# Performance work log

Hardware: AMD Instinct MI355X
Metric: run time of the kernel (lower is better)

Reference implementation:

```python
import jax, jax.numpy as jnp
import numpy as np

EPS = 1e-6
NUM_GROUPS = 32


def setup_inputs() -> dict:
    key = jax.random.key(0)
    ks = jax.random.split(key, 10)
    b, c, h, w = 8, 256, 128, 128
    x = jax.random.normal(ks[0], (b, c, h, w), dtype=jnp.float32)
    gamma = jnp.ones((c,), dtype=jnp.float32)
    beta = jnp.zeros((c,), dtype=jnp.float32)
    Wq = jax.random.normal(ks[1], (c, c), dtype=jnp.float32) * 0.02
    bq = jnp.zeros((c,), dtype=jnp.float32)
    Wk = jax.random.normal(ks[2], (c, c), dtype=jnp.float32) * 0.02
    bk = jnp.zeros((c,), dtype=jnp.float32)
    Wv = jax.random.normal(ks[3], (c, c), dtype=jnp.float32) * 0.02
    bv = jnp.zeros((c,), dtype=jnp.float32)
    Wo = jax.random.normal(ks[4], (c, c), dtype=jnp.float32) * 0.02
    bo = jnp.zeros((c,), dtype=jnp.float32)
    return {"x": x, "gamma": gamma, "beta": beta, "Wq": Wq, "bq": bq,
            "Wk": Wk, "bk": bk, "Wv": Wv, "bv": bv, "Wo": Wo, "bo": bo}


def _group_norm(x, gamma, beta):
    b, c, h, w = x.shape
    g = NUM_GROUPS
    xg = x.reshape(b, g, c // g, h, w)
    mean = jnp.mean(xg, axis=(2, 3, 4), keepdims=True)
    var = jnp.var(xg, axis=(2, 3, 4), keepdims=True)
    xn = ((xg - mean) * jax.lax.rsqrt(var + EPS)).reshape(b, c, h, w)
    return xn * gamma[None, :, None, None] + beta[None, :, None, None]


def reference(x, gamma, beta, Wq, bq, Wk, bk, Wv, bv, Wo, bo):
    b, c, h, w = x.shape
    xn = _group_norm(x, gamma, beta)
    xf = xn.reshape(b, c, h * w)  # [b, c, n]
    # 1x1 convs == channel-mixing matmuls
    Q = jnp.einsum('oc,bcn->bon', Wq, xf) + bq[None, :, None]
    K = jnp.einsum('oc,bcn->bon', Wk, xf) + bk[None, :, None]
    V = jnp.einsum('oc,bcn->bon', Wv, xf) + bv[None, :, None]
    # softmax over the spatial dim n (linear-attention variant)
    Q = jax.nn.softmax(Q, axis=-1)
    K = jax.nn.softmax(K, axis=-1)
    attn = jnp.einsum('bcn,bdn->bcd', Q, K) / jnp.sqrt(jnp.float32(c))  # [b, c, c]
    out = jnp.einsum('bcd,bdn->bcn', attn, V)  # [b, c, n]
    out = jnp.einsum('oc,bcn->bon', Wo, out) + bo[None, :, None]
    return out.reshape(b, c, h, w)
```

## Files before the change

kernel.cpp:

```cpp
#include <hip/hip_runtime.h>
#include <hip/hip_bf16.h>

#define BATCH 8
#define CHN 256
#define HWN 16384
#define EPSV 1e-6f
#define ESCH 32

typedef __attribute__((ext_vector_type(8))) short bf16x8;
typedef __attribute__((ext_vector_type(4))) short s16x4;
typedef __attribute__((ext_vector_type(4))) float f32x4;
typedef __hip_bfloat16 bf16;

__device__ __forceinline__ short f2s(float f){
  union { bf16 h; short s; } u; u.h = __float2bfloat16(f); return u.s;
}
__device__ __forceinline__ float s2f(short s){
  union { unsigned u; float f; } v; v.u = ((unsigned)(unsigned short)s) << 16; return v.f;
}
__device__ __forceinline__ void gload16(const bf16* g, bf16* l){
  __builtin_amdgcn_global_load_lds((const __attribute__((address_space(1))) void*)g,
                                   (__attribute__((address_space(3))) void*)l, 16, 0, 0);
}

__global__ __launch_bounds__(256) void xstats_t(const float* __restrict__ x,
    bf16* __restrict__ xt, float* __restrict__ pst){
  int b = blockIdx.y, n0 = blockIdx.x * 64;
  __shared__ bf16 tile[256][70];
  __shared__ float sg[32], ssg[32];
  int t = threadIdx.x;
  if (t < 32){ sg[t] = 0.f; ssg[t] = 0.f; }
  __syncthreads();
  const float* xb = x + (size_t)b * CHN * HWN;
  #pragma unroll 4
  for (int i = 0; i < 16; i++){
    int c = i * 16 + (t >> 4);
    int nf = (t & 15) * 4;
    float4 v = *(const float4*)(xb + (size_t)c * HWN + n0 + nf);
    tile[c][nf + 0] = __float2bfloat16(v.x);
    tile[c][nf + 1] = __float2bfloat16(v.y);
    tile[c][nf + 2] = __float2bfloat16(v.z);
    tile[c][nf + 3] = __float2bfloat16(v.w);
    float s  = v.x + v.y + v.z + v.w;
    float ss = v.x*v.x + v.y*v.y + v.z*v.z + v.w*v.w;
    s  += __shfl_xor(s, 1);  s  += __shfl_xor(s, 2);
    s  += __shfl_xor(s, 4);  s  += __shfl_xor(s, 8);
    ss += __shfl_xor(ss, 1); ss += __shfl_xor(ss, 2);
    ss += __shfl_xor(ss, 4); ss += __shfl_xor(ss, 8);
    if ((t & 15) == 0){ atomicAdd(&sg[c >> 3], s); atomicAdd(&ssg[c >> 3], ss); }
  }
  __syncthreads();
  bf16* o = xt + (size_t)b * HWN * CHN;
  #pragma unroll 4
  for (int j = 0; j < 64; j++)
    o[(size_t)(n0 + j) * CHN + t] = tile[t][j];
  if (t < 32){
    atomicAdd(&pst[(b * 32 + t) * 2],     sg[t]);
    atomicAdd(&pst[(b * 32 + t) * 2 + 1], ssg[t]);
  }
}

__global__ __launch_bounds__(256) void wprep(const float* __restrict__ Wq,
    const float* __restrict__ Wk, const float* __restrict__ Wv,
    const float* __restrict__ Wo, const float* __restrict__ gamma,
    const float* __restrict__ beta, const float* __restrict__ bv,
    const float* __restrict__ pst, bf16* __restrict__ wqk,
    bf16* __restrict__ wvt, bf16* __restrict__ wob, float* __restrict__ tvb){
  int w = blockIdx.x, b = blockIdx.y, rt = blockIdx.z, t = threadIdx.x;
  if (w == 3 && b != 0) return;
  const float* W = (w == 0) ? Wq : ((w == 1) ? Wk : ((w == 2) ? Wv : Wo));
  __shared__ float a_s[256], sh_s[256];
  __shared__ float racc[16];
  {
    int bg = b * 32 + (t >> 3);
    float m   = pst[bg * 2] * (1.f / 131072.f);
    float var = pst[bg * 2 + 1] * (1.f / 131072.f) - m * m;
    float r = rsqrtf(var + EPSV);
    float a = r * gamma[t];
    a_s[t] = a;
    sh_s[t] = beta[t] - m * a;
  }
  if (t < 16) racc[t] = 0.f;
  __syncthreads();
  float mya = a_s[t], mysh = sh_s[t];
  int lane = t & 63;
  bf16* wo_qk = wqk + ((size_t)b << 17) + ((size_t)w << 16);
  bf16* wo_v  = wvt + ((size_t)b << 16);
  #pragma unroll
  for (int jj = 0; jj < 16; jj++){
    int j = rt * 16 + jj;
    float wv_ = W[j * 256 + t];
    if (w < 2) wo_qk[j * 256 + t] = __float2bfloat16(wv_ * mya);
    else if (w == 3) wob[j * 256 + t] = __float2bfloat16(wv_);
    else {
      wo_v[(size_t)t * 256 + j] = __float2bfloat16(wv_ * mya);
      float p = wv_ * mysh;
      p += __shfl_xor(p, 1);  p += __shfl_xor(p, 2);  p += __shfl_xor(p, 4);
      p += __shfl_xor(p, 8);  p += __shfl_xor(p, 16); p += __shfl_xor(p, 32);
      if (lane == 0) atomicAdd(&racc[jj], p);
    }
  }
  if (w == 2){
    __syncthreads();
    if (t < 16) tvb[b * 256 + rt * 16 + t] = racc[t] + bv[rt * 16 + t];
  }
}

__global__ __launch_bounds__(256, 2) void qk_gemm(const bf16* __restrict__ wqk,
    const bf16* __restrict__ xt, bf16* __restrict__ Eout,
    float* __restrict__ sums){
  __shared__ bf16 lW[2][512 * 32];
  __shared__ bf16 lX[2][64 * 32];
  int t = threadIdx.x, nt = blockIdx.x, b = blockIdx.y;
  const bf16* Wb = wqk + ((size_t)b << 17);
  const bf16* Xb = xt + (size_t)b * HWN * CHN + (size_t)(nt * 64) * CHN;
  int lane = t & 63, w = t >> 6, r = lane & 15, kc = lane >> 4;
  f32x4 acc[4][8] = {};

  auto stage = [&](int buf, int k0){
    #pragma unroll
    for (int rep = 0; rep < 8; rep++){
      int c = t + rep * 256; int row = c >> 2;
      int off = ((c & 3) ^ ((c >> 3) & 3)) * 8;
      gload16(Wb + (size_t)row * 256 + k0 + off, &lW[buf][c * 8]);
    }
    { int row = t >> 2;
      int off = ((t & 3) ^ ((t >> 3) & 3)) * 8;
      gload16(Xb + (size_t)row * 256 + k0 + off, &lX[buf][t * 8]); }
  };

  stage(0, 0);
  __syncthreads();
  int cur = 0;
  int slot8 = (kc ^ ((r >> 1) & 3)) * 8;
  for (int ks = 0; ks < 8; ks++){
    if (ks < 7) stage(cur ^ 1, (ks + 1) * 32);
    bf16x8 af[4], bfv[8];
    #pragma unroll
    for (int i = 0; i < 4; i++)
      af[i] = *(const bf16x8*)&lX[cur][(i * 16 + r) * 32 + slot8];
    #pragma unroll
    for (int f = 0; f < 8; f++)
      bfv[f] = *(const bf16x8*)&lW[cur][(w * 128 + f * 16 + r) * 32 + slot8];
    #pragma unroll
    for (int i = 0; i < 4; i++)
      #pragma unroll
      for (int f = 0; f < 8; f++)
        acc[i][f] = __builtin_amdgcn_mfma_f32_16x16x32_bf16(af[i], bfv[f], acc[i][f], 0, 0, 0);
    __syncthreads();
    cur ^= 1;
  }

  char* scrB = (char*)&lW[0][0];
  float colp[8];
  #pragma unroll
  for (int f = 0; f < 8; f++) colp[f] = 0.f;
  #pragma unroll
  for (int f = 0; f < 8; f++){
    int wrow = w * 128 + f * 16 + r;
    int key = (wrow & 7) << 4;
    #pragma unroll
    for (int i = 0; i < 4; i++){
      s16x4 pk;
      #pragma unroll
      for (int j = 0; j < 4; j++){
        float e = __expf(acc[i][f][j]);
        colp[f] += e;
        pk[j] = f2s(e);
      }
      int nb0 = (i * 16 + kc * 4) * 2;
      *(s16x4*)(scrB + wrow * 128 + (nb0 ^ key)) = pk;
    }
  }
  #pragma unroll
  for (int f = 0; f < 8; f++){
    float v = colp[f];
    v += __shfl_xor(v, 16); v += __shfl_xor(v, 32);
    if (lane < 16){
      int wrow = w * 128 + f * 16 + r;
      int sidx = wrow < 256 ? b * 256 + wrow : 2048 + b * 256 + (wrow - 256);
      atomicAdd(&sums[sidx], v);
    }
  }
  __syncthreads();
  #pragma unroll
  for (int pass = 0; pass < 16; pass++){
    int c = t + pass * 256;
    int row = c >> 3, q = c & 7;
    int key = (row & 7) << 4;
    int4 v = *(const int4*)(scrB + row * 128 + ((q * 16) ^ key));
    size_t ridx = row < 256 ? (size_t)(b * 256 + row)
                            : (size_t)(2048 + b * 256 + row - 256);
    *(int4*)&Eout[ridx * HWN + nt * 64 + q * 8] = v;
  }
}

__global__ __launch_bounds__(256, 2) void es_gemm(const bf16* __restrict__ Ek,
    const bf16* __restrict__ Eq, float* __restrict__ spart){
  __shared__ bf16 lA[2][128 * 32];
  __shared__ bf16 lB[2][256 * 32];
  int t = threadIdx.x, ch = blockIdx.x, mt = blockIdx.y, z = blockIdx.z;
  const bf16* At = Ek + (size_t)z * 256 * HWN + (size_t)(mt * 128) * HWN + ch * 512;
  const bf16* Bt = Eq + (size_t)z * 256 * HWN + ch * 512;
  f32x4 acc[4][8] = {};
  int lane = t & 63, w = t >> 6, r = lane & 15, kc = lane >> 4;
  int ng = w >> 1, cg = w & 1;

  auto stage = [&](int buf, int k0){
    #pragma unroll
    for (int rep = 0; rep < 2; rep++){
      int c = t + rep * 256; int row = c >> 2;
      int off = ((c & 3) ^ ((c >> 3) & 3)) * 8;
      gload16(At + (size_t)row * HWN + k0 + off, &lA[buf][c * 8]);
    }
    #pragma unroll
    for (int rep = 0; rep < 4; rep++){
      int c = t + rep * 256; int row = c >> 2;
      int off = ((c & 3) ^ ((c >> 3) & 3)) * 8;
      gload16(Bt + (size_t)row * HWN + k0 + off, &lB[buf][c * 8]);
    }
  };

  stage(0, 0);
  __syncthreads();
  int cur = 0;
  int slot8 = (kc ^ ((r >> 1) & 3)) * 8;
  for (int ks = 0; ks < 16; ks++){
    if (ks < 15) stage(cur ^ 1, (ks + 1) * 32);
    bf16x8 af[4], bfv[8];
    #pragma unroll
    for (int i = 0; i < 4; i++)
      af[i] = *(const bf16x8*)&lA[cur][(ng * 64 + i * 16 + r) * 32 + slot8];
    #pragma unroll
    for (int f = 0; f < 8; f++)
      bfv[f] = *(const bf16x8*)&lB[cur][(cg * 128 + f * 16 + r) * 32 + slot8];
    #pragma unroll
    for (int i = 0; i < 4; i++)
      #pragma unroll
      for (int f = 0; f < 8; f++)
        acc[i][f] = __builtin_amdgcn_mfma_f32_16x16x32_bf16(af[i], bfv[f], acc[i][f], 0, 0, 0);
    __syncthreads();
    cur ^= 1;
  }

  float* sp = spart + ((size_t)(z * ESCH + ch) << 16);
  #pragma unroll
  for (int f = 0; f < 8; f++){
    int q = cg * 128 + f * 16 + r;
    #pragma unroll
    for (int i = 0; i < 4; i++){
      int k0i = mt * 128 + ng * 64 + i * 16 + kc * 4;
      *(f32x4*)&sp[q * 256 + k0i] = acc[i][f];
    }
  }
}

__global__ void reduce_S(const float* __restrict__ sp, float* __restrict__ S){
  size_t i = ((size_t)blockIdx.x * 256 + threadIdx.x) * 4;
  size_t b = i >> 16, cd = i & 65535;
  float4 s = {0.f, 0.f, 0.f, 0.f};
  #pragma unroll
  for (int ch = 0; ch < ESCH; ch++){
    float4 v = *(const float4*)&sp[((b * ESCH + ch) << 16) + cd];
    s.x += v.x; s.y += v.y; s.z += v.z; s.w += v.w;
  }
  *(float4*)&S[i] = s;
}

__global__ __launch_bounds__(256) void scaleS_t(const float* __restrict__ S,
    const float* __restrict__ sums, bf16* __restrict__ T1t){
  int id = blockIdx.x, b = blockIdx.y;
  int dt = id >> 2, ct = id & 3, t = threadIdx.x;
  __shared__ float tile[64][65];
  __shared__ float sq_s[64], sk_s[64];
  if (t < 64)       sq_s[t]      = 0.0625f / sums[b * 256 + ct * 64 + t];
  else if (t < 128) sk_s[t - 64] = 1.f / sums[2048 + b * 256 + dt * 64 + (t - 64)];
  const float* Sb = S + ((size_t)b << 16);
  #pragma unroll
  for (int i = 0; i < 4; i++){
    int c_l = i * 16 + (t >> 4);
    int d_l0 = (t & 15) * 4;
    float4 v = *(const float4*)&Sb[(size_t)(ct * 64 + c_l) * 256 + dt * 64 + d_l0];
    tile[d_l0 + 0][c_l] = v.x;
    tile[d_l0 + 1][c_l] = v.y;
    tile[d_l0 + 2][c_l] = v.z;
    tile[d_l0 + 3][c_l] = v.w;
  }
  __syncthreads();
  bf16* Tb = T1t + ((size_t)b << 16);
  #pragma unroll
  for (int i = 0; i < 4; i++){
    int d_l = i * 16 + (t >> 4);
    int c_l0 = (t & 15) * 4;
    s16x4 pk;
    #pragma unroll
    for (int jj = 0; jj < 4; jj++)
      pk[jj] = f2s(tile[d_l][c_l0 + jj] * sq_s[c_l0 + jj] * sk_s[d_l]);
    *(s16x4*)&Tb[(size_t)(dt * 64 + d_l) * 256 + ct * 64 + c_l0] = pk;
  }
}

__global__ __launch_bounds__(256, 2) void nt_gemm(const bf16* __restrict__ A,
    const bf16* __restrict__ B, bf16* __restrict__ out,
    long Asb, long Bsb, long Osb){
  __shared__ bf16 lA[2][256 * 32];
  __shared__ bf16 lB[2][128 * 32];
  int t = threadIdx.x, mt = blockIdx.x, b = blockIdx.y;
  const bf16* Ab = A + (size_t)b * Asb;
  const bf16* Bb = B + (size_t)b * Bsb + (size_t)(mt * 128) * 256;
  bf16* Ob = out + (size_t)b * Osb + (size_t)(mt * 128) * 256;
  int lane = t & 63, w = t >> 6, r = lane & 15, kc = lane >> 4;
  f32x4 acc[16][2] = {};

  auto stage = [&](int buf, int k0){
    #pragma unroll
    for (int rep = 0; rep < 4; rep++){
      int c = t + rep * 256; int row = c >> 2, off = (c & 3) * 8;
      gload16(Ab + (size_t)row * 256 + k0 + off, &lA[buf][c * 8]);
    }
    #pragma unroll
    for (int rep = 0; rep < 2; rep++){
      int c = t + rep * 256; int row = c >> 2, off = (c & 3) * 8;
      gload16(Bb + (size_t)row * 256 + k0 + off, &lB[buf][c * 8]);
    }
  };

  stage(0, 0);
  __syncthreads();
  int cur = 0;
  for (int ks = 0; ks < 8; ks++){
    if (ks < 7) stage(cur ^ 1, (ks + 1) * 32);
    bf16x8 bfv[2];
    #pragma unroll
    for (int f = 0; f < 2; f++)
      bfv[f] = *(const bf16x8*)&lB[cur][(w * 32 + f * 16 + r) * 32 + kc * 8];
    #pragma unroll
    for (int i = 0; i < 16; i++){
      bf16x8 af = *(const bf16x8*)&lA[cur][(i * 16 + r) * 32 + kc * 8];
      acc[i][0] = __builtin_amdgcn_mfma_f32_16x16x32_bf16(af, bfv[0], acc[i][0], 0, 0, 0);
      acc[i][1] = __builtin_amdgcn_mfma_f32_16x16x32_bf16(af, bfv[1], acc[i][1], 0, 0, 0);
    }
    __syncthreads();
    cur ^= 1;
  }

  #pragma unroll
  for (int f = 0; f < 2; f++){
    int bcol = w * 32 + f * 16 + r;
    #pragma unroll
    for (int i = 0; i < 16; i++){
      s16x4 pk;
      #pragma unroll
      for (int j = 0; j < 4; j++) pk[j] = f2s(acc[i][f][j]);
      *(s16x4*)&Ob[(size_t)bcol * 256 + i * 16 + kc * 4] = pk;
    }
  }
}

__global__ __launch_bounds__(256) void beff_k(const bf16* __restrict__ Mbf,
    const float* __restrict__ tvb, const float* __restrict__ bo,
    float* __restrict__ beff){
  int b = blockIdx.x, t = threadIdx.x;
  __shared__ float tv[256];
  tv[t] = tvb[b * 256 + t];
  __syncthreads();
  const bf16* Mr = Mbf + ((size_t)b << 16) + (size_t)t * 256;
  float s = 0.f;
  #pragma unroll
  for (int k = 0; k < 32; k++){
    bf16x8 v = *(const bf16x8*)&Mr[k * 8];
    #pragma unroll
    for (int e = 0; e < 8; e++) s += s2f(v[e]) * tv[k * 8 + e];
  }
  beff[b * 256 + t] = s + bo[t];
}

__global__ __launch_bounds__(256, 2) void out_gemm(const bf16* __restrict__ xt,
    const bf16* __restrict__ Nb, const float* __restrict__ beff,
    float* __restrict__ out){
  __shared__ bf16 lA[2][128 * 32];
  __shared__ bf16 lB[2][256 * 32];
  int t = threadIdx.x, nt = blockIdx.x, z = blockIdx.y;
  const bf16* At = xt + (size_t)z * HWN * CHN + (size_t)(nt * 128) * CHN;
  const bf16* Bt = Nb + (size_t)z * 65536;
  f32x4 acc[4][8] = {};
  int lane = t & 63, w = t >> 6, r = lane & 15, kc = lane >> 4;
  int ng = w >> 1, cg = w & 1;

  auto stage = [&](int buf, int k0){
    #pragma unroll
    for (int rep = 0; rep < 2; rep++){
      int c = t + rep * 256; int row = c >> 2;
      int off = ((c & 3) ^ ((c >> 3) & 3)) * 8;
      gload16(At + (size_t)row * 256 + k0 + off, &lA[buf][c * 8]);
    }
    #pragma unroll
    for (int rep = 0; rep < 4; rep++){
      int c = t + rep * 256; int row = c >> 2;
      int off = ((c & 3) ^ ((c >> 3) & 3)) * 8;
      gload16(Bt + (size_t)row * 256 + k0 + off, &lB[buf][c * 8]);
    }
  };

  stage(0, 0);
  __syncthreads();
  int cur = 0;
  int slot8 = (kc ^ ((r >> 1) & 3)) * 8;
  for (int ks = 0; ks < 8; ks++){
    if (ks < 7) stage(cur ^ 1, (ks + 1) * 32);
    bf16x8 af[4], bfv[8];
    #pragma unroll
    for (int i = 0; i < 4; i++)
      af[i] = *(const bf16x8*)&lA[cur][(ng * 64 + i * 16 + r) * 32 + slot8];
    #pragma unroll
    for (int f = 0; f < 8; f++)
      bfv[f] = *(const bf16x8*)&lB[cur][(cg * 128 + f * 16 + r) * 32 + slot8];
    #pragma unroll
    for (int i = 0; i < 4; i++)
      #pragma unroll
      for (int f = 0; f < 8; f++)
        acc[i][f] = __builtin_amdgcn_mfma_f32_16x16x32_bf16(af[i], bfv[f], acc[i][f], 0, 0, 0);
    __syncthreads();
    cur ^= 1;
  }

  float* ob = out + (size_t)z * CHN * HWN;
  #pragma unroll
  for (int f = 0; f < 8; f++){
    int o = cg * 128 + f * 16 + r;
    float bb = beff[z * 256 + o];
    #pragma unroll
    for (int i = 0; i < 4; i++){
      int n0 = nt * 128 + ng * 64 + i * 16 + kc * 4;
      float4 st = { acc[i][f][0] + bb, acc[i][f][1] + bb,
                    acc[i][f][2] + bb, acc[i][f][3] + bb };
      *(float4*)&ob[(size_t)o * HWN + n0] = st;
    }
  }
}

extern "C" void kernel_launch(void* const* d_in, const int* in_sizes, int n_in,
                              void* d_out, int out_size, void* d_ws, size_t ws_size,
                              hipStream_t stream){
  const float* x     = (const float*)d_in[0];
  const float* gamma = (const float*)d_in[1];
  const float* beta  = (const float*)d_in[2];
  const float* Wq    = (const float*)d_in[3];
  const float* Wk    = (const float*)d_in[5];
  const float* Wv    = (const float*)d_in[7];
  const float* bv    = (const float*)d_in[8];
  const float* Wo    = (const float*)d_in[9];
  const float* bo    = (const float*)d_in[10];

  char* ws = (char*)d_ws;
  bf16*  xt    = (bf16*) (ws + 0);
  float* spart = (float*)(ws + 67108864);
  bf16*  wqk   = (bf16*) (ws + 134217728);
  bf16*  wob   = (bf16*) (ws + 136314880);
  bf16*  wvt   = (bf16*) (ws + 136445952);
  float* S     = (float*)(ws + 137494528);
  bf16*  T1t   = (bf16*) (ws + 139591680);
  bf16*  Mbf   = (bf16*) (ws + 140640256);
  bf16*  Nb    = (bf16*) (ws + 141688832);
  float* sums  = (float*)(ws + 142737408);
  float* pst   = (float*)(ws + 142753792);
  float* tvb   = (float*)(ws + 142755840);
  float* beff  = (float*)(ws + 142764032);

  bf16* Qb = (bf16*)d_out;
  bf16* Kb = Qb + (size_t)2048 * HWN;

  hipMemsetAsync(sums, 0, 4096 * sizeof(float), stream);
  hipMemsetAsync(pst,  0,  512 * sizeof(float), stream);

  xstats_t<<<dim3(256, 8), dim3(256), 0, stream>>>(x, xt, pst);
  wprep<<<dim3(4, 8, 16), dim3(256), 0, stream>>>(Wq, Wk, Wv, Wo, gamma, beta,
                                                  bv, pst, wqk, wvt, wob, tvb);
  qk_gemm<<<dim3(256, 8), dim3(256), 0, stream>>>(wqk, xt, Qb, sums);
  es_gemm<<<dim3(ESCH, 2, 8), dim3(256), 0, stream>>>(Kb, Qb, spart);
  reduce_S<<<dim3(512), dim3(256), 0, stream>>>(spart, S);
  scaleS_t<<<dim3(16, 8), dim3(256), 0, stream>>>(S, sums, T1t);
  nt_gemm<<<dim3(2, 8), dim3(256), 0, stream>>>(T1t, wob, Mbf, 65536L, 0L, 65536L);
  beff_k<<<dim3(8), dim3(256), 0, stream>>>(Mbf, tvb, bo, beff);
  nt_gemm<<<dim3(2, 8), dim3(256), 0, stream>>>(wvt, Mbf, Nb, 65536L, 65536L, 65536L);
  out_gemm<<<dim3(128, 8), dim3(256), 0, stream>>>(xt, Nb, beff, (float*)d_out);
}
```

Baseline: 310.5 us.

## Retile qk_gemm to 256x128 blocks split over Q/K halves

The Q/K projection GEMM changes from a 512-row weight by 64-column spatial tile to a 256-row (one of Q or K) by 128-column tile, with Q/K selected by a new grid dimension. Shared memory shrinks, and each block loads half the weight per step while reusing it over twice as many spatial columns. The aim is to cut redundant weight traffic and use an LDS footprint better suited to occupancy. The exp/store epilogue becomes two passes through a smaller scratch buffer with extra barriers, and the sums atomics map to the new row layout.

```diff
diff --git a/kernel.cpp b/kernel.cpp
--- a/kernel.cpp
+++ b/kernel.cpp
@@ -109,24 +109,27 @@
 __global__ __launch_bounds__(256, 2) void qk_gemm(const bf16* __restrict__ wqk,
     const bf16* __restrict__ xt, bf16* __restrict__ Eout,
     float* __restrict__ sums){
-  __shared__ bf16 lW[2][512 * 32];
-  __shared__ bf16 lX[2][64 * 32];
-  int t = threadIdx.x, nt = blockIdx.x, b = blockIdx.y;
-  const bf16* Wb = wqk + ((size_t)b << 17);
-  const bf16* Xb = xt + (size_t)b * HWN * CHN + (size_t)(nt * 64) * CHN;
+  __shared__ bf16 lW[2][256 * 32];
+  __shared__ bf16 lX[2][128 * 32];
+  int t = threadIdx.x, nt = blockIdx.x, h = blockIdx.y, b = blockIdx.z;
+  const bf16* Wb = wqk + ((size_t)b << 17) + ((size_t)h << 16);
+  const bf16* Xb = xt + (size_t)b * HWN * CHN + (size_t)(nt * 128) * CHN;
   int lane = t & 63, w = t >> 6, r = lane & 15, kc = lane >> 4;
-  f32x4 acc[4][8] = {};
+  f32x4 acc[8][4] = {};
 
   auto stage = [&](int buf, int k0){
     #pragma unroll
-    for (int rep = 0; rep < 8; rep++){
+    for (int rep = 0; rep < 4; rep++){
       int c = t + rep * 256; int row = c >> 2;
       int off = ((c & 3) ^ ((c >> 3) & 3)) * 8;
       gload16(Wb + (size_t)row * 256 + k0 + off, &lW[buf][c * 8]);
     }
-    { int row = t >> 2;
-      int off = ((t & 3) ^ ((t >> 3) & 3)) * 8;
-      gload16(Xb + (size_t)row * 256 + k0 + off, &lX[buf][t * 8]); }
+    #pragma unroll
+    for (int rep = 0; rep < 2; rep++){
+      int c = t + rep * 256; int row = c >> 2;
+      int off = ((c & 3) ^ ((c >> 3) & 3)) * 8;
+      gload16(Xb + (size_t)row * 256 + k0 + off, &lX[buf][c * 8]);
+    }
   };
 
   stage(0, 0);
@@ -135,63 +138,62 @@
   int slot8 = (kc ^ ((r >> 1) & 3)) * 8;
   for (int ks = 0; ks < 8; ks++){
     if (ks < 7) stage(cur ^ 1, (ks + 1) * 32);
-    bf16x8 af[4], bfv[8];
-    #pragma unroll
-    for (int i = 0; i < 4; i++)
+    bf16x8 af[8], bfv[4];
+    #pragma unroll
+    for (int i = 0; i < 8; i++)
       af[i] = *(const bf16x8*)&lX[cur][(i * 16 + r) * 32 + slot8];
     #pragma unroll
-    for (int f = 0; f < 8; f++)
-      bfv[f] = *(const bf16x8*)&lW[cur][(w * 128 + f * 16 + r) * 32 + slot8];
-    #pragma unroll
-    for (int i = 0; i < 4; i++)
+    for (int f = 0; f < 4; f++)
+      bfv[f] = *(const bf16x8*)&lW[cur][(w * 64 + f * 16 + r) * 32 + slot8];
+    #pragma unroll
+    for (int i = 0; i < 8; i++)
       #pragma unroll
-      for (int f = 0; f < 8; f++)
+      for (int f = 0; f < 4; f++)
         acc[i][f] = __builtin_amdgcn_mfma_f32_16x16x32_bf16(af[i], bfv[f], acc[i][f], 0, 0, 0);
     __syncthreads();
     cur ^= 1;
   }
 
   char* scrB = (char*)&lW[0][0];
-  float colp[8];
-  #pragma unroll
-  for (int f = 0; f < 8; f++) colp[f] = 0.f;
-  #pragma unroll
-  for (int f = 0; f < 8; f++){
-    int wrow = w * 128 + f * 16 + r;
-    int key = (wrow & 7) << 4;
-    #pragma unroll
-    for (int i = 0; i < 4; i++){
-      s16x4 pk;
+  float colp[4] = {0.f, 0.f, 0.f, 0.f};
+  int base_row = (h ? 2048 : 0) + b * 256;
+  #pragma unroll
+  for (int p = 0; p < 2; p++){
+    __syncthreads();
+    #pragma unroll
+    for (int fl = 0; fl < 2; fl++){
+      int f = p * 2 + fl;
+      int ri = w * 32 + fl * 16 + r;
+      int key = (ri & 7) << 4;
       #pragma unroll
-      for (int j = 0; j < 4; j++){
-        float e = __expf(acc[i][f][j]);
-        colp[f] += e;
-        pk[j] = f2s(e);
+      for (int i = 0; i < 8; i++){
+        s16x4 pk;
+        #pragma unroll
+        for (int j = 0; j < 4; j++){
+          float e = __expf(acc[i][f][j]);
+          colp[f] += e;
+          pk[j] = f2s(e);
+        }
+        *(s16x4*)(scrB + ri * 256 + ((i * 32 + kc * 8) ^ key)) = pk;
       }
-      int nb0 = (i * 16 + kc * 4) * 2;
-      *(s16x4*)(scrB + wrow * 128 + (nb0 ^ key)) = pk;
-    }
-  }
-  #pragma unroll
-  for (int f = 0; f < 8; f++){
+    }
+    __syncthreads();
+    #pragma unroll
+    for (int ps = 0; ps < 8; ps++){
+      int c = t + ps * 256;
+      int ri = c >> 4, q = c & 15;
+      int key = (ri & 7) << 4;
+      int4 v = *(const int4*)(scrB + ri * 256 + ((q * 16) ^ key));
+      int wrow = (ri >> 5) * 64 + (p * 2 + ((ri >> 4) & 1)) * 16 + (ri & 15);
+      *(int4*)&Eout[(size_t)(base_row + wrow) * HWN + nt * 128 + q * 8] = v;
+    }
+  }
+  #pragma unroll
+  for (int f = 0; f < 4; f++){
     float v = colp[f];
     v += __shfl_xor(v, 16); v += __shfl_xor(v, 32);
-    if (lane < 16){
-      int wrow = w * 128 + f * 16 + r;
-      int sidx = wrow < 256 ? b * 256 + wrow : 2048 + b * 256 + (wrow - 256);
-      atomicAdd(&sums[sidx], v);
-    }
-  }
-  __syncthreads();
-  #pragma unroll
-  for (int pass = 0; pass < 16; pass++){
-    int c = t + pass * 256;
-    int row = c >> 3, q = c & 7;
-    int key = (row & 7) << 4;
-    int4 v = *(const int4*)(scrB + row * 128 + ((q * 16) ^ key));
-    size_t ridx = row < 256 ? (size_t)(b * 256 + row)
-                            : (size_t)(2048 + b * 256 + row - 256);
-    *(int4*)&Eout[ridx * HWN + nt * 64 + q * 8] = v;
+    if (lane < 16)
+      atomicAdd(&sums[base_row + w * 64 + f * 16 + r], v);
   }
 }
 
@@ -476,7 +478,7 @@
   xstats_t<<<dim3(256, 8), dim3(256), 0, stream>>>(x, xt, pst);
   wprep<<<dim3(4, 8, 16), dim3(256), 0, stream>>>(Wq, Wk, Wv, Wo, gamma, beta,
                                                   bv, pst, wqk, wvt, wob, tvb);
-  qk_gemm<<<dim3(256, 8), dim3(256), 0, stream>>>(wqk, xt, Qb, sums);
+  qk_gemm<<<dim3(128, 2, 8), dim3(256), 0, stream>>>(wqk, xt, Qb, sums);
   es_gemm<<<dim3(ESCH, 2, 8), dim3(256), 0, stream>>>(Kb, Qb, spart);
   reduce_S<<<dim3(512), dim3(256), 0, stream>>>(spart, S);
   scaleS_t<<<dim3(16, 8), dim3(256), 0, stream>>>(S, sums, T1t);
```

Result: faster. 293.1 us (-5.6%).
